# Kernel tuning notes

Hardware: AMD Instinct MI355X
Metric: run time of the kernel (lower is better)

Reference implementation:

```python
import jax, jax.numpy as jnp
import numpy as np

B, NA, NB, E = 2, 256, 256, 512
H1, H2 = 300, 100


def setup_inputs() -> dict:
    key = jax.random.key(0)
    ks = jax.random.split(key, 16)

    def n(k, shape, scale=1.0):
        return jax.random.normal(k, shape, dtype=jnp.float32) * scale

    z = lambda shape: jnp.zeros(shape, jnp.float32)
    return {
        "action_embedding": n(ks[0], (B, E, NA)),
        "anchor_embedding": n(ks[1], (B, E, NB)),
        "action_points": n(ks[2], (B, 3, NA)),
        "anchor_points": n(ks[3], (B, 3, NB)),
        # pairwise MLP kernel params: 2E -> 300 -> 100 -> 1
        "mlp_W1": n(ks[4], (2 * E, H1), (2 * E) ** -0.5),
        "mlp_b1": z((H1,)),
        "mlp_W2": n(ks[5], (H1, H2), H1 ** -0.5),
        "mlp_b2": z((H2,)),
        "mlp_W3": n(ks[6], (H2, 1), H2 ** -0.5),
        "mlp_b3": z((1,)),
        # PointNet [512,64,64,64,128,512] (1x1 convs) + Conv1d(512,1,bias=False)
        "pn_W0": n(ks[7], (64, 512), 512 ** -0.5),
        "pn_b0": z((64,)),
        "pn_W1": n(ks[8], (64, 64), 64 ** -0.5),
        "pn_b1": z((64,)),
        "pn_W2": n(ks[9], (64, 64), 64 ** -0.5),
        "pn_b2": z((64,)),
        "pn_W3": n(ks[10], (128, 64), 64 ** -0.5),
        "pn_b3": z((128,)),
        "pn_W4": n(ks[11], (512, 128), 128 ** -0.5),
        "pn_b4": z((512,)),
        "head_W": n(ks[12], (1, 512), 512 ** -0.5),
    }


def reference(action_embedding, anchor_embedding, action_points, anchor_points,
              mlp_W1, mlp_b1, mlp_W2, mlp_b2, mlp_W3, mlp_b3,
              pn_W0, pn_b0, pn_W1, pn_b1, pn_W2, pn_b2, pn_W3, pn_b3,
              pn_W4, pn_b4, head_W):
    P_A = action_points.transpose(0, 2, 1)      # (B, NA, 3)
    P_B = anchor_points.transpose(0, 2, 1)      # (B, NB, 3)
    Phi_A = action_embedding.transpose(0, 2, 1)  # (B, NA, E)
    Phi_B = anchor_embedding.transpose(0, 2, 1)  # (B, NB, E)
    Ed = Phi_A.shape[-1]

    # --- symmetric pairwise MLP kernel: softplus((mlp(cat(a,b)) + mlp(cat(b,a))) / 2) ---
    # First Linear layer is split so the O(NA*NB*2E) concat is never materialized:
    # cat(a,b) @ W1 == a @ W1[:E] + b @ W1[E:]
    W1a, W1b = mlp_W1[:Ed], mlp_W1[Ed:]

    def mlp_tail(h):  # h: (B, NA, NB, H1) pre-activation of layer 1
        h = jax.nn.relu(h)
        h = jax.nn.relu(h @ mlp_W2 + mlp_b2)
        return (h @ mlp_W3 + mlp_b3)[..., 0]  # (B, NA, NB)

    hA_a = Phi_A @ W1a  # (B, NA, H1)
    hA_b = Phi_A @ W1b
    hB_a = Phi_B @ W1a  # (B, NB, H1)
    hB_b = Phi_B @ W1b
    v1 = mlp_tail(hA_a[:, :, None, :] + hB_b[:, None, :, :] + mlp_b1)  # mlp(cat(x1,x2))
    v2 = mlp_tail(hB_a[:, None, :, :] + hA_b[:, :, None, :] + mlp_b1)  # mlp(cat(x2,x1))
    R_est = jax.nn.softplus((v1 + v2) * 0.5)  # (B, NA, NB) estimated distances

    # --- weighted multilateration (estimate_p), vectorized over (B, NA) ---
    # Linearized LS: ||p||^2 - 2 q_k^T p = r_k^2 - ||q_k||^2; subtract weighted means
    # to eliminate ||p||^2, then solve 3x3 weighted normal equations per action point.
    w = jnp.ones(P_B.shape[:2], R_est.dtype)            # (B, NB) uniform weights (last_attn=False)
    wsum = w.sum(-1, keepdims=True)                      # (B, 1)
    qbar = (w[..., None] * P_B).sum(1) / wsum            # (B, 3)
    bvec = (P_B ** 2).sum(-1)[:, None, :] - R_est ** 2   # (B, NA, NB)
    bbar = (w[:, None, :] * bvec).sum(-1) / wsum         # (B, NA)
    Amat = 2.0 * (P_B - qbar[:, None, :])                # (B, NB, 3)
    yvec = bvec - bbar[..., None]                        # (B, NA, NB)
    M = jnp.einsum('bki,bk,bkj->bij', Amat, w, Amat)     # (B, 3, 3)
    rhs = jnp.einsum('bki,bk,bak->bai', Amat, w, yvec)   # (B, NA, 3)
    P_A_B_pred = jnp.linalg.solve(M[:, None], rhs[..., None])[..., 0]  # (B, NA, 3)

    flow = (P_A_B_pred - P_A).transpose(0, 2, 1)         # (B, 3, NA)

    # --- PointNet flow-weight head (1x1 convs + ReLU, final conv no bias) ---
    x = action_embedding                                  # (B, 512, NA)
    for Wc, bc in ((pn_W0, pn_b0), (pn_W1, pn_b1), (pn_W2, pn_b2),
                   (pn_W3, pn_b3), (pn_W4, pn_b4)):
        x = jax.nn.relu(jnp.einsum('oi,bin->bon', Wc, x) + bc[None, :, None])
    weight = jnp.einsum('oi,bin->bon', head_W, x)        # (B, 1, NA)

    full_flow = jnp.concatenate([flow, weight], axis=1)  # (B, 4, NA)
    return full_flow
```

## Files before the change

### kernel.cpp

```cpp
#include <hip/hip_runtime.h>
#include <hip/hip_bf16.h>

typedef float f32x4 __attribute__((ext_vector_type(4)));
typedef short s16x8 __attribute__((ext_vector_type(8)));

#define OFF_EMBT   0u
#define OFF_W1T    1048576u
#define OFF_W2TSW  1662976u
#define OFF_W0BF   1734656u
#define OFF_HA     1800192u
#define OFF_R2     4421632u
#define WS_TOTAL   4945920u

__device__ __forceinline__ int pack_bf2(float a, float b) {
  __hip_bfloat162 h = __float22bfloat162_rn(make_float2(a, b));
  int r; __builtin_memcpy(&r, &h, 4); return r;
}
__device__ __forceinline__ unsigned short bf16u(float f) {
  __hip_bfloat16 h = __float2bfloat16(f);
  unsigned short u; __builtin_memcpy(&u, &h, 2); return u;
}
__device__ __forceinline__ s16x8 i4_to_s8(int a, int b, int c, int d) {
  union { int i[4]; s16x8 s; } u;
  u.i[0] = a; u.i[1] = b; u.i[2] = c; u.i[3] = d; return u.s;
}

__global__ __launch_bounds__(256) void ka_prep(
    const float* __restrict__ act_emb, const float* __restrict__ anc_emb,
    const float* __restrict__ W1, const float* __restrict__ W2,
    const float* __restrict__ W0pn, char* __restrict__ ws)
{
  __hip_bfloat16* embT  = (__hip_bfloat16*)(ws + OFF_EMBT);
  __hip_bfloat16* W1T   = (__hip_bfloat16*)(ws + OFF_W1T);
  unsigned short* W2Tsw = (unsigned short*)(ws + OFF_W2TSW);
  unsigned short* W0bf  = (unsigned short*)(ws + OFF_W0BF);
  float*          ha_ws = (float*)(ws + OFF_HA);
  __shared__ float tile[64][65];
  int blk = blockIdx.x, t = threadIdx.x;
  if (blk < 128) {
    int b = blk >> 6, emb = (blk >> 5) & 1, ntile = (blk >> 3) & 3, etile = blk & 7;
    const float* src = emb ? anc_emb : act_emb;
    int e0 = etile * 64, n0 = ntile * 64;
    int rr = t >> 6, cc = t & 63;
    #pragma unroll
    for (int it2 = 0; it2 < 16; ++it2) {
      int e_l = rr * 16 + it2;
      tile[e_l][cc] = src[(size_t)(b * 512 + e0 + e_l) * 256 + n0 + cc];
    }
    __syncthreads();
    int n_l = t >> 2, eq = t & 3;
    unsigned int* dst = (unsigned int*)(embT + ((size_t)((b * 2 + emb) * 256 + n0 + n_l)) * 512 + e0 + eq * 16);
    #pragma unroll
    for (int kk = 0; kk < 8; ++kk)
      dst[kk] = (unsigned)pack_bf2(tile[eq * 16 + 2 * kk][n_l], tile[eq * 16 + 2 * kk + 1][n_l]);
  } else if (blk < 208) {
    int id = blk - 128;
    int half = id / 40; int rem = id % 40; int et = rem / 5; int ct = rem % 5;
    int e0 = et * 64, c0 = ct * 64;
    int rr = t >> 6, cc = t & 63;
    #pragma unroll
    for (int it2 = 0; it2 < 16; ++it2) {
      int e_l = rr * 16 + it2;
      int c = c0 + cc;
      tile[e_l][cc] = (c < 300) ? W1[(size_t)(half * 512 + e0 + e_l) * 300 + c] : 0.f;
    }
    __syncthreads();
    int c_l = t >> 2, eq = t & 3;
    if (c0 + c_l < 300) {
      unsigned int* dst = (unsigned int*)(W1T + ((size_t)(half * 300 + c0 + c_l)) * 512 + e0 + eq * 16);
      #pragma unroll
      for (int kk = 0; kk < 8; ++kk)
        dst[kk] = (unsigned)pack_bf2(tile[eq * 16 + 2 * kk][c_l], tile[eq * 16 + 2 * kk + 1][c_l]);
    }
  } else if (blk < 226) {
    int idx = (blk - 208) * 256 + t;
    if (idx < 4480) {
      int nt = idx / 640; int rem = idx - nt * 640; int ks = rem >> 6; int lane = rem & 63;
      int n = nt * 16 + (lane & 15);
      int kb = ks * 32 + (lane >> 4) * 8;
      unsigned int q[4];
      #pragma unroll
      for (int jj = 0; jj < 4; ++jj) {
        int k0 = kb + jj * 2, k1 = kb + jj * 2 + 1;
        float f0 = (n < 100 && k0 < 300) ? W2[(size_t)k0 * 100 + n] : 0.f;
        float f1 = (n < 100 && k1 < 300) ? W2[(size_t)k1 * 100 + n] : 0.f;
        q[jj] = (unsigned)pack_bf2(f0, f1);
      }
      ((uint4*)W2Tsw)[idx] = make_uint4(q[0], q[1], q[2], q[3]);
    }
  } else if (blk < 242) {
    int idx = (blk - 226) * 256 + t;
    const float* s = W0pn + (size_t)idx * 8;
    ((uint4*)W0bf)[idx] = make_uint4(
        (unsigned)pack_bf2(s[0], s[1]), (unsigned)pack_bf2(s[2], s[3]),
        (unsigned)pack_bf2(s[4], s[5]), (unsigned)pack_bf2(s[6], s[7]));
  } else {
    int base = (blk - 242) * 2560;
    f32x4 z = {0.f, 0.f, 0.f, 0.f};
    #pragma unroll
    for (int r = 0; r < 10; ++r) {
      int li = base + t + 256 * r;
      int row = li / 5, cp = li % 5;
      *(f32x4*)(ha_ws + (size_t)row * 320 + 300 + cp * 4) = z;
    }
  }
}

__global__ __launch_bounds__(256) void k1_ha(
    const __hip_bfloat16* __restrict__ embT, const __hip_bfloat16* __restrict__ W1T,
    const float* __restrict__ b1, float* __restrict__ ha_ws)
{
  int blk = blockIdx.x, t = threadIdx.x;
  int b = blk / 40; int rem = blk % 40; int emb = rem / 20; rem %= 20;
  int mch = rem / 5; int nch = rem % 5;
  int wv = t >> 6, lane = t & 63, l = lane & 15, g = lane >> 4;
  const unsigned short* Ap = (const unsigned short*)embT +
      ((size_t)((b * 2 + emb) * 256 + mch * 64 + wv * 16 + l)) * 512;
  const unsigned short* Wp = (const unsigned short*)W1T;
  f32x4 z = {0.f, 0.f, 0.f, 0.f};
  f32x4 acc[8];
  #pragma unroll
  for (int nt = 0; nt < 8; ++nt) acc[nt] = z;
  for (int ks = 0; ks < 16; ++ks) {
    int k0 = ks * 32 + g * 8;
    s16x8 af = *(const s16x8*)(Ap + k0);
    #pragma unroll
    for (int nt = 0; nt < 8; ++nt) {
      int c = nch * 120 + nt * 16 + l;
      s16x8 bf = {0, 0, 0, 0, 0, 0, 0, 0};
      if (c < 600) bf = *(const s16x8*)(Wp + (size_t)c * 512 + k0);
      acc[nt] = __builtin_amdgcn_mfma_f32_16x16x32_bf16(af, bf, acc[nt], 0, 0, 0);
    }
  }
  #pragma unroll
  for (int nt = 0; nt < 8; ++nt) {
    int cl = nt * 16 + l;
    int c = nch * 120 + cl;
    if (cl < 120 && c < 600) {
      int half = (c >= 300) ? 1 : 0;
      int cc = c - half * 300;
      float bias = (emb == 0) ? b1[cc] : 0.f;
      float* Dp = ha_ws + ((size_t)((b * 4 + emb * 2 + half) * 256 + mch * 64 + wv * 16)) * 320 + cc;
      #pragma unroll
      for (int r = 0; r < 4; ++r)
        Dp[(size_t)(g * 4 + r) * 320] = acc[nt][r] + bias;
    }
  }
}

union KSM {
  int4 w2s[3840];
  unsigned short xbuf[16 * 520];
};

template<int K, int NT>
__device__ __forceinline__ void pn_layer(unsigned short* xb, const float* __restrict__ W,
                                         const float* __restrict__ bias, int wv, int l, int g)
{
  constexpr int NN = NT / 4;
  f32x4 z = {0.f, 0.f, 0.f, 0.f};
  f32x4 acc[NN];
  #pragma unroll
  for (int nn = 0; nn < NN; ++nn) acc[nn] = z;
  #pragma unroll
  for (int nn = 0; nn < NN; ++nn) {
    int o = (wv + nn * 4) * 16 + l;
    const float* wr0 = W + (size_t)o * K;
    #pragma unroll
    for (int ks = 0; ks < K / 32; ++ks) {
      int koff = ks * 32 + g * 8;
      f32x4 wa = *(const f32x4*)(wr0 + koff);
      f32x4 wb = *(const f32x4*)(wr0 + koff + 4);
      s16x8 bfr = i4_to_s8(pack_bf2(wa.x, wa.y), pack_bf2(wa.z, wa.w),
                           pack_bf2(wb.x, wb.y), pack_bf2(wb.z, wb.w));
      s16x8 a0 = *(const s16x8*)(xb + (size_t)l * 520 + koff);
      acc[nn] = __builtin_amdgcn_mfma_f32_16x16x32_bf16(a0, bfr, acc[nn], 0, 0, 0);
    }
  }
  __syncthreads();
  #pragma unroll
  for (int nn = 0; nn < NN; ++nn) {
    int chan = (wv + nn * 4) * 16 + l;
    float bv = bias[chan];
    #pragma unroll
    for (int r = 0; r < 4; ++r)
      xb[(size_t)(g * 4 + r) * 520 + chan] = bf16u(fmaxf(acc[nn][r] + bv, 0.f));
  }
  __syncthreads();
}

__global__ __launch_bounds__(256, 2) void k2_main(
    const float* __restrict__ ha_ws, const unsigned short* __restrict__ W2Tsw,
    const float* __restrict__ b2g, const float* __restrict__ W3g, const float* __restrict__ b3g,
    float* __restrict__ R2,
    const __hip_bfloat16* __restrict__ embT, const unsigned short* __restrict__ W0bf,
    const float* __restrict__ pnW1, const float* __restrict__ pnW2,
    const float* __restrict__ pnW3, const float* __restrict__ pnW4,
    const float* __restrict__ pnB0, const float* __restrict__ pnB1,
    const float* __restrict__ pnB2, const float* __restrict__ pnB3,
    const float* __restrict__ pnB4,
    const float* __restrict__ headW, float* __restrict__ out)
{
  __shared__ KSM sm;
  int blk = blockIdx.x, t = threadIdx.x;
  int wv = t >> 6, lane = t & 63, l = lane & 15, g = lane >> 4;
  int b = blk >> 8, it = (blk >> 4) & 15, jt = blk & 15;
  int i0 = it * 16, j0 = jt * 16;
  {
    const int4* w2g = (const int4*)W2Tsw;
    for (int u = t; u < 3840; u += 256) sm.w2s[u] = w2g[u];
  }
  __syncthreads();
  float w3v[7], b2v[7];
  #pragma unroll
  for (int nt = 0; nt < 7; ++nt) {
    int n = nt * 16 + l;
    w3v[nt] = (n < 100) ? W3g[n] : 0.f;
    b2v[nt] = (n < 100) ? b2g[n] : 0.f;
  }
  float vsum[16];
  #pragma unroll
  for (int q = 0; q < 16; ++q) vsum[q] = 0.f;
  #pragma unroll 1
  for (int rep = 0; rep < 2; ++rep) {
    const float* hap = ha_ws + ((size_t)((b * 4 + rep) * 256 + i0 + l)) * 320;
    const float* hbp = ha_ws + ((size_t)((b * 4 + (rep ? 2 : 3)) * 256 + j0 + wv * 4)) * 320;
    f32x4 z = {0.f, 0.f, 0.f, 0.f};
    f32x4 acc[4][7];
    #pragma unroll
    for (int mt = 0; mt < 4; ++mt)
      #pragma unroll
      for (int nt = 0; nt < 7; ++nt) acc[mt][nt] = z;
    for (int ks = 0; ks < 10; ++ks) {
      int koff = ks * 32 + g * 8;
      s16x8 bf[7];
      #pragma unroll
      for (int nt = 0; nt < 6; ++nt)
        bf[nt] = *(const s16x8*)&sm.w2s[(nt * 10 + ks) * 64 + lane];
      bf[6] = *(const s16x8*)(W2Tsw + ((size_t)(60 + ks) * 64 + lane) * 8);
      f32x4 ha0 = *(const f32x4*)(hap + koff);
      f32x4 ha1 = *(const f32x4*)(hap + koff + 4);
      #pragma unroll
      for (int mt = 0; mt < 4; ++mt) {
        const float* hb = hbp + (size_t)mt * 320 + koff;
        f32x4 hb0 = *(const f32x4*)hb;
        f32x4 hb1 = *(const f32x4*)(hb + 4);
        s16x8 af = i4_to_s8(
            pack_bf2(fmaxf(ha0.x + hb0.x, 0.f), fmaxf(ha0.y + hb0.y, 0.f)),
            pack_bf2(fmaxf(ha0.z + hb0.z, 0.f), fmaxf(ha0.w + hb0.w, 0.f)),
            pack_bf2(fmaxf(ha1.x + hb1.x, 0.f), fmaxf(ha1.y + hb1.y, 0.f)),
            pack_bf2(fmaxf(ha1.z + hb1.z, 0.f), fmaxf(ha1.w + hb1.w, 0.f)));
        #pragma unroll
        for (int nt = 0; nt < 7; ++nt)
          acc[mt][nt] = __builtin_amdgcn_mfma_f32_16x16x32_bf16(af, bf[nt], acc[mt][nt], 0, 0, 0);
      }
    }
    #pragma unroll
    for (int mt = 0; mt < 4; ++mt)
      #pragma unroll
      for (int r = 0; r < 4; ++r) {
        float pv = 0.f;
        #pragma unroll
        for (int nt = 0; nt < 7; ++nt)
          pv += fmaxf(acc[mt][nt][r] + b2v[nt], 0.f) * w3v[nt];
        vsum[mt * 4 + r] += pv;
      }
  }
  {
    float b3 = b3g[0];
    #pragma unroll
    for (int mt = 0; mt < 4; ++mt)
      #pragma unroll
      for (int r = 0; r < 4; ++r) {
        float s = vsum[mt * 4 + r];
        s += __shfl_xor(s, 1);
        s += __shfl_xor(s, 2);
        s += __shfl_xor(s, 4);
        s += __shfl_xor(s, 8);
        float S = 0.5f * s + b3;
        float Rr = (S > 20.f) ? S : log1pf(expf(S));
        if (l == 0) {
          int ii = i0 + g * 4 + r, jj2 = j0 + wv * 4 + mt;
          R2[((size_t)(b * 256 + ii)) * 256 + jj2] = Rr * Rr;
        }
      }
  }
  if (blk < 32) {
    __syncthreads();
    int b_pn = blk >> 4, n0 = (blk & 15) * 16;
    unsigned short* xb = sm.xbuf;
    {
      const unsigned short* A0 = (const unsigned short*)embT + ((size_t)(b_pn * 2 * 256 + n0)) * 512;
      f32x4 acc0 = {0.f, 0.f, 0.f, 0.f};
      int o = wv * 16 + l;
      const unsigned short* w0r = W0bf + (size_t)o * 512;
      #pragma unroll
      for (int ks = 0; ks < 16; ++ks) {
        int koff = ks * 32 + g * 8;
        s16x8 bfr = *(const s16x8*)(w0r + koff);
        s16x8 a0 = *(const s16x8*)(A0 + (size_t)l * 512 + koff);
        acc0 = __builtin_amdgcn_mfma_f32_16x16x32_bf16(a0, bfr, acc0, 0, 0, 0);
      }
      float bv = pnB0[o];
      #pragma unroll
      for (int r = 0; r < 4; ++r)
        xb[(size_t)(g * 4 + r) * 520 + o] = bf16u(fmaxf(acc0[r] + bv, 0.f));
      __syncthreads();
    }
    pn_layer<64, 4>(xb, pnW1, pnB1, wv, l, g);
    pn_layer<64, 4>(xb, pnW2, pnB2, wv, l, g);
    pn_layer<64, 8>(xb, pnW3, pnB3, wv, l, g);
    pn_layer<128, 32>(xb, pnW4, pnB4, wv, l, g);
    {
      int p_l = t >> 4, os = t & 15;
      const unsigned short* row = xb + (size_t)p_l * 520 + os * 32;
      float s = 0.f;
      #pragma unroll
      for (int c = 0; c < 32; ++c) {
        unsigned int u = ((unsigned int)row[c]) << 16;
        float xv; __builtin_memcpy(&xv, &u, 4);
        s += xv * headW[os * 32 + c];
      }
      s += __shfl_xor(s, 1); s += __shfl_xor(s, 2);
      s += __shfl_xor(s, 4); s += __shfl_xor(s, 8);
      if (os == 0) out[(size_t)(b_pn * 4 + 3) * 256 + n0 + p_l] = s;
    }
  }
}

__device__ __forceinline__ float block_sum(float v, float* redbuf, int t) {
  #pragma unroll
  for (int m = 1; m < 64; m <<= 1) v += __shfl_xor(v, m);
  __syncthreads();
  if ((t & 63) == 0) redbuf[t >> 6] = v;
  __syncthreads();
  return redbuf[0] + redbuf[1] + redbuf[2] + redbuf[3];
}

__global__ __launch_bounds__(256) void k3_solve(
    const float* __restrict__ anc_pts, const float* __restrict__ act_pts,
    const float* __restrict__ R2, float* __restrict__ out)
{
  __shared__ float Ax[256], Ay[256], Az[256];
  __shared__ float redbuf[4];
  int blk = blockIdx.x, t = threadIdx.x;
  int b = blk >> 2, ic = blk & 3;
  int k = t;
  float px = anc_pts[(size_t)(b * 3 + 0) * 256 + k];
  float py = anc_pts[(size_t)(b * 3 + 1) * 256 + k];
  float pz = anc_pts[(size_t)(b * 3 + 2) * 256 + k];
  float qx = block_sum(px, redbuf, t) * (1.f / 256.f);
  float qy = block_sum(py, redbuf, t) * (1.f / 256.f);
  float qz = block_sum(pz, redbuf, t) * (1.f / 256.f);
  float ax = 2.f * (px - qx), ay = 2.f * (py - qy), az = 2.f * (pz - qz);
  float p2 = px * px + py * py + pz * pz;
  Ax[k] = ax; Ay[k] = ay; Az[k] = az;
  float mxx = block_sum(ax * ax, redbuf, t);
  float mxy = block_sum(ax * ay, redbuf, t);
  float mxz = block_sum(ax * az, redbuf, t);
  float myy = block_sum(ay * ay, redbuf, t);
  float myz = block_sum(ay * az, redbuf, t);
  float mzz = block_sum(az * az, redbuf, t);
  float c0x = block_sum(ax * p2, redbuf, t);
  float c0y = block_sum(ay * p2, redbuf, t);
  float c0z = block_sum(az * p2, redbuf, t);
  __syncthreads();
  float det = mxx * (myy * mzz - myz * myz) - mxy * (mxy * mzz - myz * mxz) + mxz * (mxy * myz - myy * mxz);
  float idet = 1.f / det;
  float i00 = (myy * mzz - myz * myz) * idet;
  float i01 = (mxz * myz - mxy * mzz) * idet;
  float i02 = (mxy * myz - mxz * myy) * idet;
  float i11 = (mxx * mzz - mxz * mxz) * idet;
  float i12 = (mxy * mxz - mxx * myz) * idet;
  float i22 = (mxx * myy - mxy * mxy) * idet;
  int il = t >> 2, ks = t & 3;
  int i = ic * 64 + il;
  const float* rrow = R2 + ((size_t)(b * 256 + i)) * 256;
  float r0 = 0.f, r1 = 0.f, r2 = 0.f;
  #pragma unroll
  for (int kk = 0; kk < 16; ++kk) {
    int kb = ks * 64 + kk * 4;
    f32x4 rv = *(const f32x4*)(rrow + kb);
    r0 += Ax[kb] * rv.x + Ax[kb + 1] * rv.y + Ax[kb + 2] * rv.z + Ax[kb + 3] * rv.w;
    r1 += Ay[kb] * rv.x + Ay[kb + 1] * rv.y + Ay[kb + 2] * rv.z + Ay[kb + 3] * rv.w;
    r2 += Az[kb] * rv.x + Az[kb + 1] * rv.y + Az[kb + 2] * rv.z + Az[kb + 3] * rv.w;
  }
  r0 += __shfl_xor(r0, 1); r0 += __shfl_xor(r0, 2);
  r1 += __shfl_xor(r1, 1); r1 += __shfl_xor(r1, 2);
  r2 += __shfl_xor(r2, 1); r2 += __shfl_xor(r2, 2);
  if (ks == 0) {
    float hx = c0x - r0, hy = c0y - r1, hz = c0z - r2;
    float x0 = i00 * hx + i01 * hy + i02 * hz;
    float x1 = i01 * hx + i11 * hy + i12 * hz;
    float x2 = i02 * hx + i12 * hy + i22 * hz;
    out[(size_t)(b * 4 + 0) * 256 + i] = x0 - act_pts[(size_t)(b * 3 + 0) * 256 + i];
    out[(size_t)(b * 4 + 1) * 256 + i] = x1 - act_pts[(size_t)(b * 3 + 1) * 256 + i];
    out[(size_t)(b * 4 + 2) * 256 + i] = x2 - act_pts[(size_t)(b * 3 + 2) * 256 + i];
  }
}

extern "C" void kernel_launch(void* const* d_in, const int* in_sizes, int n_in,
                              void* d_out, int out_size, void* d_ws, size_t ws_size,
                              hipStream_t stream)
{
  const float* act_emb = (const float*)d_in[0];
  const float* anc_emb = (const float*)d_in[1];
  const float* act_pts = (const float*)d_in[2];
  const float* anc_pts = (const float*)d_in[3];
  const float* W1  = (const float*)d_in[4];
  const float* b1  = (const float*)d_in[5];
  const float* W2  = (const float*)d_in[6];
  const float* b2  = (const float*)d_in[7];
  const float* W3  = (const float*)d_in[8];
  const float* b3  = (const float*)d_in[9];
  const float* pnW0 = (const float*)d_in[10];
  const float* pnB0 = (const float*)d_in[11];
  const float* pnW1 = (const float*)d_in[12];
  const float* pnB1 = (const float*)d_in[13];
  const float* pnW2 = (const float*)d_in[14];
  const float* pnB2 = (const float*)d_in[15];
  const float* pnW3 = (const float*)d_in[16];
  const float* pnB3 = (const float*)d_in[17];
  const float* pnW4 = (const float*)d_in[18];
  const float* pnB4 = (const float*)d_in[19];
  const float* headW = (const float*)d_in[20];
  char* ws = (char*)d_ws;
  __hip_bfloat16* embT  = (__hip_bfloat16*)(ws + OFF_EMBT);
  __hip_bfloat16* W1T   = (__hip_bfloat16*)(ws + OFF_W1T);
  unsigned short* W2Tsw = (unsigned short*)(ws + OFF_W2TSW);
  unsigned short* W0bf  = (unsigned short*)(ws + OFF_W0BF);
  float* ha_ws = (float*)(ws + OFF_HA);
  float* R2ws  = (float*)(ws + OFF_R2);
  float* outp  = (float*)d_out;

  ka_prep<<<246, 256, 0, stream>>>(act_emb, anc_emb, W1, W2, pnW0, ws);
  k1_ha<<<80, 256, 0, stream>>>(embT, W1T, b1, ha_ws);
  k2_main<<<512, 256, 0, stream>>>(ha_ws, W2Tsw, b2, W3, b3, R2ws, embT, W0bf,
                                   pnW1, pnW2, pnW3, pnW4, pnB0, pnB1, pnB2, pnB3, pnB4,
                                   headW, outp);
  k3_solve<<<8, 256, 0, stream>>>(anc_pts, act_pts, R2ws, outp);
}
```

Measured before the change: 182.1 us.

## Move PointNet head into k1 and split pairwise MLP into smaller tiles

The PointNet head leaves the tail of the pairwise-MLP kernel and runs as extra blocks in the layer-1 projection kernel, whose grid grows from 80 to 320 finer blocks with two column tiles per wave. The pairwise kernel now uses 8-column j tiles across 1024 blocks, holds less W2 in LDS and allows 4 blocks per CU, which is meant to raise occupancy and remove the serial PointNet tail. In exchange, each block reloads W2 and h_a rows for half as many pairs, so redundant global traffic goes up.

Result: slower. 370.7 us (+103.6%).

```diff
diff --git a/kernel.cpp b/kernel.cpp
--- a/kernel.cpp
+++ b/kernel.cpp
@@ -106,53 +106,6 @@
   }
 }
 
-__global__ __launch_bounds__(256) void k1_ha(
-    const __hip_bfloat16* __restrict__ embT, const __hip_bfloat16* __restrict__ W1T,
-    const float* __restrict__ b1, float* __restrict__ ha_ws)
-{
-  int blk = blockIdx.x, t = threadIdx.x;
-  int b = blk / 40; int rem = blk % 40; int emb = rem / 20; rem %= 20;
-  int mch = rem / 5; int nch = rem % 5;
-  int wv = t >> 6, lane = t & 63, l = lane & 15, g = lane >> 4;
-  const unsigned short* Ap = (const unsigned short*)embT +
-      ((size_t)((b * 2 + emb) * 256 + mch * 64 + wv * 16 + l)) * 512;
-  const unsigned short* Wp = (const unsigned short*)W1T;
-  f32x4 z = {0.f, 0.f, 0.f, 0.f};
-  f32x4 acc[8];
-  #pragma unroll
-  for (int nt = 0; nt < 8; ++nt) acc[nt] = z;
-  for (int ks = 0; ks < 16; ++ks) {
-    int k0 = ks * 32 + g * 8;
-    s16x8 af = *(const s16x8*)(Ap + k0);
-    #pragma unroll
-    for (int nt = 0; nt < 8; ++nt) {
-      int c = nch * 120 + nt * 16 + l;
-      s16x8 bf = {0, 0, 0, 0, 0, 0, 0, 0};
-      if (c < 600) bf = *(const s16x8*)(Wp + (size_t)c * 512 + k0);
-      acc[nt] = __builtin_amdgcn_mfma_f32_16x16x32_bf16(af, bf, acc[nt], 0, 0, 0);
-    }
-  }
-  #pragma unroll
-  for (int nt = 0; nt < 8; ++nt) {
-    int cl = nt * 16 + l;
-    int c = nch * 120 + cl;
-    if (cl < 120 && c < 600) {
-      int half = (c >= 300) ? 1 : 0;
-      int cc = c - half * 300;
-      float bias = (emb == 0) ? b1[cc] : 0.f;
-      float* Dp = ha_ws + ((size_t)((b * 4 + emb * 2 + half) * 256 + mch * 64 + wv * 16)) * 320 + cc;
-      #pragma unroll
-      for (int r = 0; r < 4; ++r)
-        Dp[(size_t)(g * 4 + r) * 320] = acc[nt][r] + bias;
-    }
-  }
-}
-
-union KSM {
-  int4 w2s[3840];
-  unsigned short xbuf[16 * 520];
-};
-
 template<int K, int NT>
 __device__ __forceinline__ void pn_layer(unsigned short* xb, const float* __restrict__ W,
                                          const float* __restrict__ bias, int wv, int l, int g)
@@ -189,11 +142,10 @@
   __syncthreads();
 }
 
-__global__ __launch_bounds__(256, 2) void k2_main(
-    const float* __restrict__ ha_ws, const unsigned short* __restrict__ W2Tsw,
-    const float* __restrict__ b2g, const float* __restrict__ W3g, const float* __restrict__ b3g,
-    float* __restrict__ R2,
-    const __hip_bfloat16* __restrict__ embT, const unsigned short* __restrict__ W0bf,
+__global__ __launch_bounds__(256) void k1_ha(
+    const __hip_bfloat16* __restrict__ embT, const __hip_bfloat16* __restrict__ W1T,
+    const float* __restrict__ b1, float* __restrict__ ha_ws,
+    const unsigned short* __restrict__ W0bf,
     const float* __restrict__ pnW1, const float* __restrict__ pnW2,
     const float* __restrict__ pnW3, const float* __restrict__ pnW4,
     const float* __restrict__ pnB0, const float* __restrict__ pnB1,
@@ -201,14 +153,99 @@
     const float* __restrict__ pnB4,
     const float* __restrict__ headW, float* __restrict__ out)
 {
-  __shared__ KSM sm;
+  __shared__ unsigned short xbuf[16 * 520];
   int blk = blockIdx.x, t = threadIdx.x;
   int wv = t >> 6, lane = t & 63, l = lane & 15, g = lane >> 4;
-  int b = blk >> 8, it = (blk >> 4) & 15, jt = blk & 15;
-  int i0 = it * 16, j0 = jt * 16;
+  if (blk < 320) {
+    int b = blk / 160; int r = blk % 160; int emb = r / 80; r %= 80;
+    int mch = r / 5; int nch = r % 5;
+    int m0 = mch * 16;
+    const unsigned short* Ap = (const unsigned short*)embT +
+        ((size_t)((b * 2 + emb) * 256 + m0 + l)) * 512;
+    const unsigned short* Wp = (const unsigned short*)W1T;
+    f32x4 z = {0.f, 0.f, 0.f, 0.f};
+    f32x4 acc[2] = {z, z};
+    for (int ks = 0; ks < 16; ++ks) {
+      int k0 = ks * 32 + g * 8;
+      s16x8 af = *(const s16x8*)(Ap + k0);
+      #pragma unroll
+      for (int q = 0; q < 2; ++q) {
+        int c = nch * 120 + (wv * 2 + q) * 16 + l;
+        s16x8 bf = {0, 0, 0, 0, 0, 0, 0, 0};
+        if (c < 600) bf = *(const s16x8*)(Wp + (size_t)c * 512 + k0);
+        acc[q] = __builtin_amdgcn_mfma_f32_16x16x32_bf16(af, bf, acc[q], 0, 0, 0);
+      }
+    }
+    #pragma unroll
+    for (int q = 0; q < 2; ++q) {
+      int cl = (wv * 2 + q) * 16 + l;
+      int c = nch * 120 + cl;
+      if (cl < 120 && c < 600) {
+        int half = (c >= 300) ? 1 : 0;
+        int cc = c - half * 300;
+        float bias = (emb == 0) ? b1[cc] : 0.f;
+        float* Dp = ha_ws + ((size_t)((b * 4 + emb * 2 + half) * 256 + m0 + g * 4)) * 320 + cc;
+        #pragma unroll
+        for (int r2 = 0; r2 < 4; ++r2)
+          Dp[(size_t)r2 * 320] = acc[q][r2] + bias;
+      }
+    }
+  } else {
+    int pn = blk - 320;
+    int b_pn = pn >> 4, n0 = (pn & 15) * 16;
+    unsigned short* xb = xbuf;
+    {
+      const unsigned short* A0 = (const unsigned short*)embT + ((size_t)(b_pn * 2 * 256 + n0)) * 512;
+      f32x4 acc0 = {0.f, 0.f, 0.f, 0.f};
+      int o = wv * 16 + l;
+      const unsigned short* w0r = W0bf + (size_t)o * 512;
+      #pragma unroll
+      for (int ks = 0; ks < 16; ++ks) {
+        int koff = ks * 32 + g * 8;
+        s16x8 bfr = *(const s16x8*)(w0r + koff);
+        s16x8 a0 = *(const s16x8*)(A0 + (size_t)l * 512 + koff);
+        acc0 = __builtin_amdgcn_mfma_f32_16x16x32_bf16(a0, bfr, acc0, 0, 0, 0);
+      }
+      float bv = pnB0[o];
+      #pragma unroll
+      for (int r2 = 0; r2 < 4; ++r2)
+        xb[(size_t)(g * 4 + r2) * 520 + o] = bf16u(fmaxf(acc0[r2] + bv, 0.f));
+      __syncthreads();
+    }
+    pn_layer<64, 4>(xb, pnW1, pnB1, wv, l, g);
+    pn_layer<64, 4>(xb, pnW2, pnB2, wv, l, g);
+    pn_layer<64, 8>(xb, pnW3, pnB3, wv, l, g);
+    pn_layer<128, 32>(xb, pnW4, pnB4, wv, l, g);
+    {
+      int p_l = t >> 4, os = t & 15;
+      const unsigned short* row = xb + (size_t)p_l * 520 + os * 32;
+      float s = 0.f;
+      #pragma unroll
+      for (int c = 0; c < 32; ++c) {
+        unsigned int u = ((unsigned int)row[c]) << 16;
+        float xv; __builtin_memcpy(&xv, &u, 4);
+        s += xv * headW[os * 32 + c];
+      }
+      s += __shfl_xor(s, 1); s += __shfl_xor(s, 2);
+      s += __shfl_xor(s, 4); s += __shfl_xor(s, 8);
+      if (os == 0) out[(size_t)(b_pn * 4 + 3) * 256 + n0 + p_l] = s;
+    }
+  }
+}
+
+__global__ __launch_bounds__(256, 4) void k2_main(
+    const float* __restrict__ ha_ws, const unsigned short* __restrict__ W2Tsw,
+    const float* __restrict__ b2g, const float* __restrict__ W3g, const float* __restrict__ b3g,
+    float* __restrict__ R2)
+{
+  __shared__ int4 w2s[2560];
+  int blk = blockIdx.x, t = threadIdx.x;
+  int wv = t >> 6, lane = t & 63, l = lane & 15, g = lane >> 4;
+  int b = blk >> 9, it = (blk >> 5) & 15, jt = blk & 31;
+  int i0 = it * 16, j0 = jt * 8;
   {
     const int4* w2g = (const int4*)W2Tsw;
-    for (int u = t; u < 3840; u += 256) sm.w2s[u] = w2g[u];
+    for (int u = t; u < 2560; u += 256) w2s[u] = w2g[u];
   }
   __syncthreads();
   float w3v[7], b2v[7];
@@ -218,45 +255,48 @@
     w3v[nt] = (n < 100) ? W3g[n] : 0.f;
     b2v[nt] = (n < 100) ? b2g[n] : 0.f;
   }
-  float vsum[16];
-  #pragma unroll
-  for (int q = 0; q < 16; ++q) vsum[q] = 0.f;
+  float vsum[8];
+  #pragma unroll
+  for (int q = 0; q < 8; ++q) vsum[q] = 0.f;
   #pragma unroll 1
   for (int rep = 0; rep < 2; ++rep) {
     const float* hap = ha_ws + ((size_t)((b * 4 + rep) * 256 + i0 + l)) * 320;
-    const float* hbp = ha_ws + ((size_t)((b * 4 + (rep ? 2 : 3)) * 256 + j0 + wv * 4)) * 320;
+    const float* hbp = ha_ws + ((size_t)((b * 4 + (rep ? 2 : 3)) * 256 + j0 + wv * 2)) * 320;
     f32x4 z = {0.f, 0.f, 0.f, 0.f};
-    f32x4 acc[4][7];
-    #pragma unroll
-    for (int mt = 0; mt < 4; ++mt)
+    f32x4 acc[2][7];
+    #pragma unroll
+    for (int mt = 0; mt < 2; ++mt)
       #pragma unroll
       for (int nt = 0; nt < 7; ++nt) acc[mt][nt] = z;
     for (int ks = 0; ks < 10; ++ks) {
       int koff = ks * 32 + g * 8;
       s16x8 bf[7];
       #pragma unroll
-      for (int nt = 0; nt < 6; ++nt)
-        bf[nt] = *(const s16x8*)&sm.w2s[(nt * 10 + ks) * 64 + lane];
-      bf[6] = *(const s16x8*)(W2Tsw + ((size_t)(60 + ks) * 64 + lane) * 8);
+      for (int nt = 0; nt < 4; ++nt)
+        bf[nt] = *(const s16x8*)&w2s[(nt * 10 + ks) * 64 + lane];
+      #pragma unroll
+      for (int nt = 4; nt < 7; ++nt)
+        bf[nt] = *(const s16x8*)(W2Tsw + ((size_t)(nt * 10 + ks) * 64 + lane) * 8);
       f32x4 ha0 = *(const f32x4*)(hap + koff);
       f32x4 ha1 = *(const f32x4*)(hap + koff + 4);
       #pragma unroll
-      for (int mt = 0; mt < 4; ++mt) {
+      for (int mt = 0; mt < 2; ++mt) {
         const float* hb = hbp + (size_t)mt * 320 + koff;
         f32x4 hb0 = *(const f32x4*)hb;
         f32x4 hb1 = *(const f32x4*)(hb + 4);
-        s16x8 af = i4_to_s8(
-            pack_bf2(fmaxf(ha0.x + hb0.x, 0.f), fmaxf(ha0.y + hb0.y, 0.f)),
-            pack_bf2(fmaxf(ha0.z + hb0.z, 0.f), fmaxf(ha0.w + hb0.w, 0.f)),
-            pack_bf2(fmaxf(ha1.x + hb1.x, 0.f), fmaxf(ha1.y + hb1.y, 0.f)),
-            pack_bf2(fmaxf(ha1.z + hb1.z, 0.f), fmaxf(ha1.w + hb1.w, 0.f)));
+        f32x4 s0 = ha0 + hb0;
+        f32x4 s1 = ha1 + hb1;
+        s0 = __builtin_elementwise_max(s0, z);
+        s1 = __builtin_elementwise_max(s1, z);
+        s16x8 af = i4_to_s8(pack_bf2(s0.x, s0.y), pack_bf2(s0.z, s0.w),
+                            pack_bf2(s1.x, s1.y), pack_bf2(s1.z, s1.w));
         #pragma unroll
         for (int nt = 0; nt < 7; ++nt)
           acc[mt][nt] = __builtin_amdgcn_mfma_f32_16x16x32_bf16(af, bf[nt], acc[mt][nt], 0, 0, 0);
       }
     }
     #pragma unroll
-    for (int mt = 0; mt < 4; ++mt)
+    for (int mt = 0; mt < 2; ++mt)
       #pragma unroll
       for (int r = 0; r < 4; ++r) {
         float pv = 0.f;
@@ -269,7 +309,7 @@
   {
     float b3 = b3g[0];
     #pragma unroll
-    for (int mt = 0; mt < 4; ++mt)
+    for (int mt = 0; mt < 2; ++mt)
       #pragma unroll
       for (int r = 0; r < 4; ++r) {
         float s = vsum[mt * 4 + r];
@@ -280,51 +320,10 @@
         float S = 0.5f * s + b3;
         float Rr = (S > 20.f) ? S : log1pf(expf(S));
         if (l == 0) {
-          int ii = i0 + g * 4 + r, jj2 = j0 + wv * 4 + mt;
+          int ii = i0 + g * 4 + r, jj2 = j0 + wv * 2 + mt;
           R2[((size_t)(b * 256 + ii)) * 256 + jj2] = Rr * Rr;
         }
       }
-  }
-  if (blk < 32) {
-    __syncthreads();
-    int b_pn = blk >> 4, n0 = (blk & 15) * 16;
-    unsigned short* xb = sm.xbuf;
-    {
-      const unsigned short* A0 = (const unsigned short*)embT + ((size_t)(b_pn * 2 * 256 + n0)) * 512;
-      f32x4 acc0 = {0.f, 0.f, 0.f, 0.f};
-      int o = wv * 16 + l;
-      const unsigned short* w0r = W0bf + (size_t)o * 512;
-      #pragma unroll
-      for (int ks = 0; ks < 16; ++ks) {
-        int koff = ks * 32 + g * 8;
-        s16x8 bfr = *(const s16x8*)(w0r + koff);
-        s16x8 a0 = *(const s16x8*)(A0 + (size_t)l * 512 + koff);
-        acc0 = __builtin_amdgcn_mfma_f32_16x16x32_bf16(a0, bfr, acc0, 0, 0, 0);
-      }
-      float bv = pnB0[o];
-      #pragma unroll
-      for (int r = 0; r < 4; ++r)
-        xb[(size_t)(g * 4 + r) * 520 + o] = bf16u(fmaxf(acc0[r] + bv, 0.f));
-      __syncthreads();
-    }
-    pn_layer<64, 4>(xb, pnW1, pnB1, wv, l, g);
-    pn_layer<64, 4>(xb, pnW2, pnB2, wv, l, g);
-    pn_layer<64, 8>(xb, pnW3, pnB3, wv, l, g);
-    pn_layer<128, 32>(xb, pnW4, pnB4, wv, l, g);
-    {
-      int p_l = t >> 4, os = t & 15;
-      const unsigned short* row = xb + (size_t)p_l * 520 + os * 32;
-      float s = 0.f;
-      #pragma unroll
-      for (int c = 0; c < 32; ++c) {
-        unsigned int u = ((unsigned int)row[c]) << 16;
-        float xv; __builtin_memcpy(&xv, &u, 4);
-        s += xv * headW[os * 32 + c];
-      }
-      s += __shfl_xor(s, 1); s += __shfl_xor(s, 2);
-      s += __shfl_xor(s, 4); s += __shfl_xor(s, 8);
-      if (os == 0) out[(size_t)(b_pn * 4 + 3) * 256 + n0 + p_l] = s;
-    }
   }
 }
 
@@ -434,9 +433,9 @@
   float* outp  = (float*)d_out;
 
   ka_prep<<<246, 256, 0, stream>>>(act_emb, anc_emb, W1, W2, pnW0, ws);
-  k1_ha<<<80, 256, 0, stream>>>(embT, W1T, b1, ha_ws);
-  k2_main<<<512, 256, 0, stream>>>(ha_ws, W2Tsw, b2, W3, b3, R2ws, embT, W0bf,
-                                   pnW1, pnW2, pnW3, pnW4, pnB0, pnB1, pnB2, pnB3, pnB4,
-                                   headW, outp);
+  k1_ha<<<352, 256, 0, stream>>>(embT, W1T, b1, ha_ws, W0bf,
+                                 pnW1, pnW2, pnW3, pnW4, pnB0, pnB1, pnB2, pnB3, pnB4,
+                                 headW, outp);
+  k2_main<<<1024, 256, 0, stream>>>(ha_ws, W2Tsw, b2, W3, b3, R2ws);
   k3_solve<<<8, 256, 0, stream>>>(anc_pts, act_pts, R2ws, outp);
 }
```
